# Kernel tuning notes

Measured on AMD Instinct MI355X. Metric: run time of the kernel, lower is better.

The kernel has to match this reference:

```python
import jax, jax.numpy as jnp
import numpy as np

B, N, G = 32, 1024, 8   # batch, Nvecs (= k_in), Nglobals
K_OUT, H = 128, 128     # MLP output width, hidden width
D_IN = 1 + N + G        # MLP input width: [u, norm, dots]


def setup_inputs() -> dict:
    key = jax.random.key(0)
    ks = jax.random.split(key, 8)
    x = jax.random.uniform(ks[0], (B, N, 3), dtype=jnp.float32)  # positive coords -> dots >= 0
    u = jax.random.normal(ks[1], (B, G), dtype=jnp.float32)
    s0 = 1.0 / np.sqrt(D_IN)
    s1 = 1.0 / np.sqrt(H)
    W0 = jax.random.normal(ks[2], (D_IN, H), dtype=jnp.float32) * s0
    b0 = jnp.zeros((H,), dtype=jnp.float32)
    W1 = jax.random.normal(ks[3], (H, H), dtype=jnp.float32) * s1
    b1 = jnp.zeros((H,), dtype=jnp.float32)
    W2 = jax.random.normal(ks[4], (H, K_OUT), dtype=jnp.float32) * s1
    b2 = jnp.zeros((K_OUT,), dtype=jnp.float32)
    return {"x": x, "u": u, "W0": W0, "b0": b0, "W1": W1, "b1": b1, "W2": W2, "b2": b2}


def reference(x, u, W0, b0, W1, b1, W2, b2):
    # x: [B, N, 3], u: [B, G]
    norms = jnp.linalg.norm(x, axis=-1, keepdims=True)            # [B, N, 1]
    dots = jnp.sqrt(jnp.einsum('bid,bjd->bij', x, x))             # [B, N, N]
    u_rep = jnp.broadcast_to(u[:, None, :], (x.shape[0], x.shape[1], u.shape[-1]))
    scalars = jnp.concatenate([u_rep, norms, dots], axis=-1)      # [B, N, G+1+N]
    # MLP (Linear -> LeakyReLU -> Linear -> LeakyReLU -> Linear)
    h = jax.nn.leaky_relu(scalars @ W0 + b0)
    h = jax.nn.leaky_relu(h @ W1 + b1)
    fk = h @ W2 + b2                                              # [B, N, K_OUT]
    # outer product 'bio,bid->biod' followed by mean over i == fused contraction
    out = jnp.einsum('bio,bid->bod', fk, x) / x.shape[1]          # [B, K_OUT, 3]
    return out
```

## Files before the change

kernel.cpp:

```cpp
#include <hip/hip_runtime.h>
#include <hip/hip_fp16.h>

typedef _Float16 f16;
typedef f16 f16x4 __attribute__((ext_vector_type(4)));
typedef f16 f16x8 __attribute__((ext_vector_type(8)));
typedef float f32x4 __attribute__((ext_vector_type(4)));

#define NN 1024

#define IMG2_OFF  0
#define W8_OFF    327680
#define BIAS0_OFF 328192

__global__ __launch_bounds__(256) void prep_kernel(
    const float* __restrict__ u,  const float* __restrict__ W0,
    const float* __restrict__ b0, const float* __restrict__ W1,
    const float* __restrict__ W2,
    f16* __restrict__ img2, float* __restrict__ w8v, float* __restrict__ bias0,
    float* __restrict__ outp)
{
    const int t = threadIdx.x;
    const int blk = blockIdx.x;
    if (blk < 160) {
        int flat = blk * 1024 + t * 4;
        int c   = flat >> 13;
        int rem = flat & 8191;
        int s0  = rem & 7;
        int lm  = (rem >> 3) & 15;
        int q   = (rem >> 7) & 3;
        int ks  = (rem >> 9) & 1;
        int nt  = (rem >> 10) & 3;
        int wn  = (rem >> 12) & 1;
        int n = wn * 64 + nt * 16 + lm;
        f16x4 v;
#pragma unroll
        for (int e = 0; e < 4; ++e) {
            int k = ks * 32 + q * 8 + s0 + e;
            float val;
            if (c < 16)       val = W0[(9 + c * 64 + k) * 128 + n];
            else if (c < 18)  val = W1[((c - 16) * 64 + k) * 128 + n];
            else              val = W2[((c - 18) * 64 + k) * 128 + n];
            v[e] = (f16)val;
        }
        *(f16x4*)&img2[flat] = v;
    } else if (blk < 176) {
        int idx = (blk - 160) * 256 + t;
        int b = idx >> 7, h = idx & 127;
        float s = b0[h];
#pragma unroll
        for (int g = 0; g < 8; ++g) s += u[b * 8 + g] * W0[g * 128 + h];
        bias0[idx] = s;
    } else if (blk == 176) {
        if (t < 128) w8v[t] = W0[8 * 128 + t];
    } else {
        int idx = (blk - 177) * 1024 + t * 4;
        if (idx < 12288) { float4 z = {0.f, 0.f, 0.f, 0.f}; *(float4*)&outp[idx] = z; }
    }
}

__global__ __launch_bounds__(256, 4) void fused_kernel(
    const float* __restrict__ x, const float* __restrict__ b1p,
    const float* __restrict__ b2p, const f16* __restrict__ img2,
    const float* __restrict__ w8v, const float* __restrict__ bias0,
    float* __restrict__ outp)
{
    __shared__ __align__(16) f16 Dsh[2][64 * 64];
    __shared__ __align__(16) f16 xjsh[1024 * 4];
    __shared__ __align__(16) float xi[64 * 4];
    __shared__ float normv[64];
    __shared__ float biass[128];
    __shared__ float w8s[128];

    const int t = threadIdx.x;
    const int b = blockIdx.x >> 4;
    const int i0 = (blockIdx.x & 15) * 64;

    {
        const float* xb = x + (size_t)b * NN * 3;
        float4 v0 = *(const float4*)(xb + t * 12);
        float4 v1 = *(const float4*)(xb + t * 12 + 4);
        float4 v2 = *(const float4*)(xb + t * 12 + 8);
        f16x4 r0; r0[0] = (f16)v0.x; r0[1] = (f16)v0.y; r0[2] = (f16)v0.z; r0[3] = (f16)0;
        f16x4 r1; r1[0] = (f16)v0.w; r1[1] = (f16)v1.x; r1[2] = (f16)v1.y; r1[3] = (f16)0;
        f16x4 r2; r2[0] = (f16)v1.z; r2[1] = (f16)v1.w; r2[2] = (f16)v2.x; r2[3] = (f16)0;
        f16x4 r3; r3[0] = (f16)v2.y; r3[1] = (f16)v2.z; r3[2] = (f16)v2.w; r3[3] = (f16)0;
        *(f16x4*)&xjsh[(t * 4 + 0) * 4] = r0;
        *(f16x4*)&xjsh[(t * 4 + 1) * 4] = r1;
        *(f16x4*)&xjsh[(t * 4 + 2) * 4] = r2;
        *(f16x4*)&xjsh[(t * 4 + 3) * 4] = r3;
    }
    if (t < 192) {
        int i = t / 3, d = t - i * 3;
        xi[i * 4 + d] = x[(size_t)(b * NN + i0 + i) * 3 + d];
    }
    if (t < 128) { biass[t] = bias0[b * 128 + t]; w8s[t] = w8v[t]; }
    __syncthreads();
    if (t < 64) {
        float a0 = xi[t * 4], a1 = xi[t * 4 + 1], a2 = xi[t * 4 + 2];
        normv[t] = __builtin_amdgcn_sqrtf(a0 * a0 + a1 * a1 + a2 * a2);
    }

    const int lane = t & 63, wv = t >> 6;
    const int wm = wv >> 1, wn = wv & 1;
    const int lm = lane & 15, q = lane >> 4;

    f16x4 bi[4];
#pragma unroll
    for (int it = 0; it < 4; ++it) {
        f16x4 v; v[0] = (f16)0; v[1] = (f16)0; v[2] = (f16)0; v[3] = (f16)0;
        if (q == 0) {
            int ii = it * 16 + lm;
            v[0] = (f16)xi[ii * 4];
            v[1] = (f16)xi[ii * 4 + 1];
            v[2] = (f16)xi[ii * 4 + 2];
        }
        bi[it] = v;
    }

    f32x4 acc[2][4];
    auto zero_acc = [&]() {
#pragma unroll
        for (int mt = 0; mt < 2; ++mt)
#pragma unroll
            for (int nt = 0; nt < 4; ++nt)
#pragma unroll
                for (int e = 0; e < 4; ++e) acc[mt][nt][e] = 0.f;
    };
    zero_acc();

    auto dotstore = [&](int jc, int buf) {
        f16x4 ajv; ajv[0] = (f16)0; ajv[1] = (f16)0; ajv[2] = (f16)0; ajv[3] = (f16)0;
        if (q == 0)
            ajv = *(const f16x4*)&xjsh[(jc * 64 + wv * 16 + lm) * 4];
        f32x4 cg[4];
#pragma unroll
        for (int it = 0; it < 4; ++it) {
            f32x4 z; z[0] = 0.f; z[1] = 0.f; z[2] = 0.f; z[3] = 0.f;
            cg[it] = __builtin_amdgcn_mfma_f32_16x16x16f16(ajv, bi[it], z, 0, 0, 0);
        }
#pragma unroll
        for (int it = 0; it < 4; ++it) {
            f16x4 dv;
#pragma unroll
            for (int r = 0; r < 4; ++r)
                dv[r] = (f16)__builtin_amdgcn_sqrtf(fmaxf(cg[it][r], 0.f));
            int row = it * 16 + lm;
            int colstart = wv * 16 + q * 4;
            int addr = row * 64 + (((colstart & ~7) ^ ((row & 7) << 3)) | (colstart & 7));
            *(f16x4*)&Dsh[buf][addr] = dv;
        }
    };

    auto kstep = [&](int dbuf, int c, int dotjc, int dotbuf) {
        f16x8 af[2][2];
#pragma unroll
        for (int mt = 0; mt < 2; ++mt)
#pragma unroll
            for (int ks = 0; ks < 2; ++ks) {
                int row = wm * 32 + mt * 16 + lm;
                int col = ks * 32 + q * 8;
                af[mt][ks] = *(const f16x8*)(Dsh[dbuf] + row * 64 + (col ^ ((row & 7) << 3)));
            }
        const f16* wb = img2 + (size_t)(c * 2 + wn) * 4096 + lane * 8;
        f16x8 bf[4][2];
#pragma unroll
        for (int nt = 0; nt < 4; ++nt)
#pragma unroll
            for (int ks = 0; ks < 2; ++ks)
                bf[nt][ks] = *(const f16x8*)(wb + (nt * 2 + ks) * 512);
        if (dotjc >= 0) dotstore(dotjc, dotbuf);
#pragma unroll
        for (int ks = 0; ks < 2; ++ks)
#pragma unroll
            for (int mt = 0; mt < 2; ++mt)
#pragma unroll
                for (int nt = 0; nt < 4; ++nt)
                    acc[mt][nt] = __builtin_amdgcn_mfma_f32_16x16x32_f16(
                        af[mt][ks], bf[nt][ks], acc[mt][nt], 0, 0, 0);
    };

    dotstore(0, 0);
    __syncthreads();

#pragma unroll
    for (int jc = 0; jc < 16; ++jc) {
        const int cur = jc & 1, nxt = cur ^ 1;
        kstep(cur, jc, (jc < 15) ? jc + 1 : -1, nxt);
        __syncthreads();
    }

#pragma unroll
    for (int mt = 0; mt < 2; ++mt)
#pragma unroll
        for (int nt = 0; nt < 4; ++nt) {
            const int h = wn * 64 + nt * 16 + lm;
            const float bh = biass[h], w8h = w8s[h];
            const int hh = h & 63;
#pragma unroll
            for (int r = 0; r < 4; ++r) {
                int i = wm * 32 + mt * 16 + q * 4 + r;
                float val = acc[mt][nt][r] + bh + normv[i] * w8h;
                val = val > 0.f ? val : 0.01f * val;
                int addr = i * 64 + (((hh & ~7) ^ ((i & 7) << 3)) | (hh & 7));
                Dsh[wn][addr] = (f16)val;
            }
        }
    __syncthreads();

    zero_acc();
    kstep(0, 16, -1, 0);
    kstep(1, 17, -1, 0);
    __syncthreads();

#pragma unroll
    for (int mt = 0; mt < 2; ++mt)
#pragma unroll
        for (int nt = 0; nt < 4; ++nt) {
            const int h = wn * 64 + nt * 16 + lm;
            const float bh = b1p[h];
            const int hh = h & 63;
#pragma unroll
            for (int r = 0; r < 4; ++r) {
                int i = wm * 32 + mt * 16 + q * 4 + r;
                float val = acc[mt][nt][r] + bh;
                val = val > 0.f ? val : 0.01f * val;
                int addr = i * 64 + (((hh & ~7) ^ ((i & 7) << 3)) | (hh & 7));
                Dsh[wn][addr] = (f16)val;
            }
        }
    __syncthreads();

    zero_acc();
    kstep(0, 18, -1, 0);
    kstep(1, 19, -1, 0);

    float p[4][3];
#pragma unroll
    for (int nt = 0; nt < 4; ++nt)
#pragma unroll
        for (int d = 0; d < 3; ++d) p[nt][d] = 0.f;
    float bo[4];
#pragma unroll
    for (int nt = 0; nt < 4; ++nt) bo[nt] = b2p[wn * 64 + nt * 16 + lm];
#pragma unroll
    for (int mt = 0; mt < 2; ++mt)
#pragma unroll
        for (int r = 0; r < 4; ++r) {
            int i = wm * 32 + mt * 16 + q * 4 + r;
            float x0 = xi[i * 4], x1 = xi[i * 4 + 1], x2 = xi[i * 4 + 2];
#pragma unroll
            for (int nt = 0; nt < 4; ++nt) {
                float fkv = acc[mt][nt][r] + bo[nt];
                p[nt][0] = fmaf(fkv, x0, p[nt][0]);
                p[nt][1] = fmaf(fkv, x1, p[nt][1]);
                p[nt][2] = fmaf(fkv, x2, p[nt][2]);
            }
        }
#pragma unroll
    for (int nt = 0; nt < 4; ++nt)
#pragma unroll
        for (int d = 0; d < 3; ++d) {
            float s = p[nt][d];
            s += __shfl_xor(s, 16);
            s += __shfl_xor(s, 32);
            if (q == 0) {
                int o = wn * 64 + nt * 16 + lm;
                atomicAdd(&outp[(b * 128 + o) * 3 + d], s * (1.0f / 1024.0f));
            }
        }
}

extern "C" void kernel_launch(void* const* d_in, const int* in_sizes, int n_in,
                              void* d_out, int out_size, void* d_ws, size_t ws_size,
                              hipStream_t stream) {
    const float* x  = (const float*)d_in[0];
    const float* u  = (const float*)d_in[1];
    const float* W0 = (const float*)d_in[2];
    const float* b0 = (const float*)d_in[3];
    const float* W1 = (const float*)d_in[4];
    const float* b1 = (const float*)d_in[5];
    const float* W2 = (const float*)d_in[6];
    const float* b2 = (const float*)d_in[7];

    char* ws = (char*)d_ws;
    f16*   img2  = (f16*)(ws + IMG2_OFF);
    float* w8v   = (float*)(ws + W8_OFF);
    float* bias0 = (float*)(ws + BIAS0_OFF);
    float* out   = (float*)d_out;

    prep_kernel<<<189, 256, 0, stream>>>(u, W0, b0, W1, W2, img2, w8v, bias0, out);
    fused_kernel<<<512, 256, 0, stream>>>(x, b1, b2, img2, w8v, bias0, out);
}
```

Before: 93.00 us.

## Repartition waves over N, prefetch weight tiles, and keep hidden layers in one LDS tile

Each of the four waves now owns a 32-column slice of the hidden dimension across all 64 rows, instead of a 2x2 grid of 32x64 tiles. Weight fragments for the next j-chunk are double-buffered in registers and loaded before the current MFMAs, and the layer-1/2 weights are loaded before the preceding epilogue. Layers 1 and 2 run as a single K=128 pass over a 64x128 LDS tile rather than two K=64 kstep calls. The aim is to hide global weight-load latency. In exchange the kernel uses more registers, so launch bounds drop to 2 blocks per SIMD, which lowers occupancy.

```diff
diff --git a/kernel.cpp b/kernel.cpp
--- a/kernel.cpp
+++ b/kernel.cpp
@@ -58,7 +58,7 @@
     }
 }
 
-__global__ __launch_bounds__(256, 4) void fused_kernel(
+__global__ __launch_bounds__(256, 2) void fused_kernel(
     const float* __restrict__ x, const float* __restrict__ b1p,
     const float* __restrict__ b2p, const f16* __restrict__ img2,
     const float* __restrict__ w8v, const float* __restrict__ bias0,
@@ -74,6 +74,12 @@
     const int t = threadIdx.x;
     const int b = blockIdx.x >> 4;
     const int i0 = (blockIdx.x & 15) * 64;
+
+    const int lane = t & 63, wv = t >> 6;
+    const int lm = lane & 15, q = lane >> 4;
+    const int half = wv >> 1;
+    const int nbase = (wv & 1) * 2;
+    f16* Hh = &Dsh[0][0];
 
     {
         const float* xb = x + (size_t)b * NN * 3;
@@ -100,10 +106,6 @@
         normv[t] = __builtin_amdgcn_sqrtf(a0 * a0 + a1 * a1 + a2 * a2);
     }
 
-    const int lane = t & 63, wv = t >> 6;
-    const int wm = wv >> 1, wn = wv & 1;
-    const int lm = lane & 15, q = lane >> 4;
-
     f16x4 bi[4];
 #pragma unroll
     for (int it = 0; it < 4; ++it) {
@@ -117,33 +119,18 @@
         bi[it] = v;
     }
 
-    f32x4 acc[2][4];
-    auto zero_acc = [&]() {
-#pragma unroll
-        for (int mt = 0; mt < 2; ++mt)
-#pragma unroll
-            for (int nt = 0; nt < 4; ++nt)
-#pragma unroll
-                for (int e = 0; e < 4; ++e) acc[mt][nt][e] = 0.f;
-    };
-    zero_acc();
-
     auto dotstore = [&](int jc, int buf) {
         f16x4 ajv; ajv[0] = (f16)0; ajv[1] = (f16)0; ajv[2] = (f16)0; ajv[3] = (f16)0;
         if (q == 0)
             ajv = *(const f16x4*)&xjsh[(jc * 64 + wv * 16 + lm) * 4];
-        f32x4 cg[4];
 #pragma unroll
         for (int it = 0; it < 4; ++it) {
             f32x4 z; z[0] = 0.f; z[1] = 0.f; z[2] = 0.f; z[3] = 0.f;
-            cg[it] = __builtin_amdgcn_mfma_f32_16x16x16f16(ajv, bi[it], z, 0, 0, 0);
-        }
-#pragma unroll
-        for (int it = 0; it < 4; ++it) {
+            f32x4 cg = __builtin_amdgcn_mfma_f32_16x16x16f16(ajv, bi[it], z, 0, 0, 0);
             f16x4 dv;
 #pragma unroll
             for (int r = 0; r < 4; ++r)
-                dv[r] = (f16)__builtin_amdgcn_sqrtf(fmaxf(cg[it][r], 0.f));
+                dv[r] = (f16)__builtin_amdgcn_sqrtf(fmaxf(cg[r], 0.f));
             int row = it * 16 + lm;
             int colstart = wv * 16 + q * 4;
             int addr = row * 64 + (((colstart & ~7) ^ ((row & 7) << 3)) | (colstart & 7));
@@ -151,120 +138,187 @@
         }
     };
 
-    auto kstep = [&](int dbuf, int c, int dotjc, int dotbuf) {
-        f16x8 af[2][2];
-#pragma unroll
-        for (int mt = 0; mt < 2; ++mt)
-#pragma unroll
-            for (int ks = 0; ks < 2; ++ks) {
-                int row = wm * 32 + mt * 16 + lm;
-                int col = ks * 32 + q * 8;
-                af[mt][ks] = *(const f16x8*)(Dsh[dbuf] + row * 64 + (col ^ ((row & 7) << 3)));
-            }
-        const f16* wb = img2 + (size_t)(c * 2 + wn) * 4096 + lane * 8;
-        f16x8 bf[4][2];
-#pragma unroll
-        for (int nt = 0; nt < 4; ++nt)
+    f32x4 acc[4][2];
+    auto zero_acc = [&]() {
+#pragma unroll
+        for (int mt = 0; mt < 4; ++mt)
+#pragma unroll
+            for (int n2 = 0; n2 < 2; ++n2)
+#pragma unroll
+                for (int e = 0; e < 4; ++e) acc[mt][n2][e] = 0.f;
+    };
+    zero_acc();
+
+    f16x8 bfbuf[2][2][2];
+    {
+        const f16* wb = img2 + (size_t)(0 * 2 + half) * 4096 + lane * 8;
+#pragma unroll
+        for (int n2 = 0; n2 < 2; ++n2)
 #pragma unroll
             for (int ks = 0; ks < 2; ++ks)
-                bf[nt][ks] = *(const f16x8*)(wb + (nt * 2 + ks) * 512);
-        if (dotjc >= 0) dotstore(dotjc, dotbuf);
-#pragma unroll
-        for (int ks = 0; ks < 2; ++ks)
-#pragma unroll
-            for (int mt = 0; mt < 2; ++mt)
-#pragma unroll
-                for (int nt = 0; nt < 4; ++nt)
-                    acc[mt][nt] = __builtin_amdgcn_mfma_f32_16x16x32_f16(
-                        af[mt][ks], bf[nt][ks], acc[mt][nt], 0, 0, 0);
-    };
-
+                bfbuf[0][n2][ks] = *(const f16x8*)(wb + (((nbase + n2) * 2 + ks)) * 512);
+    }
     dotstore(0, 0);
     __syncthreads();
 
 #pragma unroll
     for (int jc = 0; jc < 16; ++jc) {
         const int cur = jc & 1, nxt = cur ^ 1;
-        kstep(cur, jc, (jc < 15) ? jc + 1 : -1, nxt);
+        if (jc < 15) {
+            const f16* wb = img2 + (size_t)((jc + 1) * 2 + half) * 4096 + lane * 8;
+#pragma unroll
+            for (int n2 = 0; n2 < 2; ++n2)
+#pragma unroll
+                for (int ks = 0; ks < 2; ++ks)
+                    bfbuf[nxt][n2][ks] = *(const f16x8*)(wb + (((nbase + n2) * 2 + ks)) * 512);
+        }
+        f16x8 af[4][2];
+#pragma unroll
+        for (int mt = 0; mt < 4; ++mt)
+#pragma unroll
+            for (int ks = 0; ks < 2; ++ks) {
+                int row = mt * 16 + lm;
+                int col = ks * 32 + q * 8;
+                af[mt][ks] = *(const f16x8*)(Dsh[cur] + row * 64 + (col ^ ((row & 7) << 3)));
+            }
+        if (jc < 15) dotstore(jc + 1, nxt);
+#pragma unroll
+        for (int ks = 0; ks < 2; ++ks)
+#pragma unroll
+            for (int mt = 0; mt < 4; ++mt)
+#pragma unroll
+                for (int n2 = 0; n2 < 2; ++n2)
+                    acc[mt][n2] = __builtin_amdgcn_mfma_f32_16x16x32_f16(
+                        af[mt][ks], bfbuf[cur][n2][ks], acc[mt][n2], 0, 0, 0);
         __syncthreads();
     }
 
-#pragma unroll
-    for (int mt = 0; mt < 2; ++mt)
-#pragma unroll
-        for (int nt = 0; nt < 4; ++nt) {
-            const int h = wn * 64 + nt * 16 + lm;
+    f16x8 bL[2][4];
+#pragma unroll
+    for (int n2 = 0; n2 < 2; ++n2)
+#pragma unroll
+        for (int ks = 0; ks < 4; ++ks) {
+            const f16* wb = img2 + (size_t)((16 + (ks >> 1)) * 2 + half) * 4096 + lane * 8;
+            bL[n2][ks] = *(const f16x8*)(wb + (((nbase + n2) * 2 + (ks & 1))) * 512);
+        }
+
+#pragma unroll
+    for (int mt = 0; mt < 4; ++mt)
+#pragma unroll
+        for (int n2 = 0; n2 < 2; ++n2) {
+            const int h = wv * 32 + n2 * 16 + lm;
             const float bh = biass[h], w8h = w8s[h];
-            const int hh = h & 63;
 #pragma unroll
             for (int r = 0; r < 4; ++r) {
-                int i = wm * 32 + mt * 16 + q * 4 + r;
-                float val = acc[mt][nt][r] + bh + normv[i] * w8h;
+                int i = mt * 16 + q * 4 + r;
+                float val = acc[mt][n2][r] + bh + normv[i] * w8h;
                 val = val > 0.f ? val : 0.01f * val;
-                int addr = i * 64 + (((hh & ~7) ^ ((i & 7) << 3)) | (hh & 7));
-                Dsh[wn][addr] = (f16)val;
+                int addr = i * 128 + (((h & ~7) ^ ((i & 7) << 3)) | (h & 7));
+                Hh[addr] = (f16)val;
             }
         }
     __syncthreads();
 
     zero_acc();
-    kstep(0, 16, -1, 0);
-    kstep(1, 17, -1, 0);
-    __syncthreads();
-
-#pragma unroll
-    for (int mt = 0; mt < 2; ++mt)
-#pragma unroll
-        for (int nt = 0; nt < 4; ++nt) {
-            const int h = wn * 64 + nt * 16 + lm;
+    {
+        f16x8 af[4][4];
+#pragma unroll
+        for (int mt = 0; mt < 4; ++mt)
+#pragma unroll
+            for (int ks = 0; ks < 4; ++ks) {
+                int row = mt * 16 + lm;
+                int col = ks * 32 + q * 8;
+                af[mt][ks] = *(const f16x8*)(Hh + row * 128 + (col ^ ((row & 7) << 3)));
+            }
+#pragma unroll
+        for (int ks = 0; ks < 4; ++ks)
+#pragma unroll
+            for (int mt = 0; mt < 4; ++mt)
+#pragma unroll
+                for (int n2 = 0; n2 < 2; ++n2)
+                    acc[mt][n2] = __builtin_amdgcn_mfma_f32_16x16x32_f16(
+                        af[mt][ks], bL[n2][ks], acc[mt][n2], 0, 0, 0);
+    }
+
+    f16x8 bM[2][4];
+#pragma unroll
+    for (int n2 = 0; n2 < 2; ++n2)
+#pragma unroll
+        for (int ks = 0; ks < 4; ++ks) {
+            const f16* wb = img2 + (size_t)((18 + (ks >> 1)) * 2 + half) * 4096 + lane * 8;
+            bM[n2][ks] = *(const f16x8*)(wb + (((nbase + n2) * 2 + (ks & 1))) * 512);
+        }
+    __syncthreads();
+
+#pragma unroll
+    for (int mt = 0; mt < 4; ++mt)
+#pragma unroll
+        for (int n2 = 0; n2 < 2; ++n2) {
+            const int h = wv * 32 + n2 * 16 + lm;
             const float bh = b1p[h];
-            const int hh = h & 63;
 #pragma unroll
             for (int r = 0; r < 4; ++r) {
-                int i = wm * 32 + mt * 16 + q * 4 + r;
-                float val = acc[mt][nt][r] + bh;
+                int i = mt * 16 + q * 4 + r;
+                float val = acc[mt][n2][r] + bh;
                 val = val > 0.f ? val : 0.01f * val;
-                int addr = i * 64 + (((hh & ~7) ^ ((i & 7) << 3)) | (hh & 7));
-                Dsh[wn][addr] = (f16)val;
+                int addr = i * 128 + (((h & ~7) ^ ((i & 7) << 3)) | (h & 7));
+                Hh[addr] = (f16)val;
             }
         }
     __syncthreads();
 
     zero_acc();
-    kstep(0, 18, -1, 0);
-    kstep(1, 19, -1, 0);
-
-    float p[4][3];
-#pragma unroll
-    for (int nt = 0; nt < 4; ++nt)
-#pragma unroll
-        for (int d = 0; d < 3; ++d) p[nt][d] = 0.f;
-    float bo[4];
-#pragma unroll
-    for (int nt = 0; nt < 4; ++nt) bo[nt] = b2p[wn * 64 + nt * 16 + lm];
-#pragma unroll
-    for (int mt = 0; mt < 2; ++mt)
+    {
+        f16x8 af[4][4];
+#pragma unroll
+        for (int mt = 0; mt < 4; ++mt)
+#pragma unroll
+            for (int ks = 0; ks < 4; ++ks) {
+                int row = mt * 16 + lm;
+                int col = ks * 32 + q * 8;
+                af[mt][ks] = *(const f16x8*)(Hh + row * 128 + (col ^ ((row & 7) << 3)));
+            }
+#pragma unroll
+        for (int ks = 0; ks < 4; ++ks)
+#pragma unroll
+            for (int mt = 0; mt < 4; ++mt)
+#pragma unroll
+                for (int n2 = 0; n2 < 2; ++n2)
+                    acc[mt][n2] = __builtin_amdgcn_mfma_f32_16x16x32_f16(
+                        af[mt][ks], bM[n2][ks], acc[mt][n2], 0, 0, 0);
+    }
+
+    float p[2][3];
+#pragma unroll
+    for (int n2 = 0; n2 < 2; ++n2)
+#pragma unroll
+        for (int d = 0; d < 3; ++d) p[n2][d] = 0.f;
+    float bo[2];
+#pragma unroll
+    for (int n2 = 0; n2 < 2; ++n2) bo[n2] = b2p[wv * 32 + n2 * 16 + lm];
+#pragma unroll
+    for (int mt = 0; mt < 4; ++mt)
 #pragma unroll
         for (int r = 0; r < 4; ++r) {
-            int i = wm * 32 + mt * 16 + q * 4 + r;
+            int i = mt * 16 + q * 4 + r;
             float x0 = xi[i * 4], x1 = xi[i * 4 + 1], x2 = xi[i * 4 + 2];
 #pragma unroll
-            for (int nt = 0; nt < 4; ++nt) {
-                float fkv = acc[mt][nt][r] + bo[nt];
-                p[nt][0] = fmaf(fkv, x0, p[nt][0]);
-                p[nt][1] = fmaf(fkv, x1, p[nt][1]);
-                p[nt][2] = fmaf(fkv, x2, p[nt][2]);
-            }
-        }
-#pragma unroll
-    for (int nt = 0; nt < 4; ++nt)
+            for (int n2 = 0; n2 < 2; ++n2) {
+                float fkv = acc[mt][n2][r] + bo[n2];
+                p[n2][0] = fmaf(fkv, x0, p[n2][0]);
+                p[n2][1] = fmaf(fkv, x1, p[n2][1]);
+                p[n2][2] = fmaf(fkv, x2, p[n2][2]);
+            }
+        }
+#pragma unroll
+    for (int n2 = 0; n2 < 2; ++n2)
 #pragma unroll
         for (int d = 0; d < 3; ++d) {
-            float s = p[nt][d];
+            float s = p[n2][d];
             s += __shfl_xor(s, 16);
             s += __shfl_xor(s, 32);
             if (q == 0) {
-                int o = wn * 64 + nt * 16 + lm;
+                int o = wv * 32 + n2 * 16 + lm;
                 atomicAdd(&outp[(b * 128 + o) * 3 + d], s * (1.0f / 1024.0f));
             }
         }
```

Measured after the change: 85.44 us. 1.09x faster.

## Give each wave private dot tiles to remove per-chunk block barriers

Applied to the files above, without the earlier changes.

Each wave now computes its own 32x64 slice of sqrt-dot values into a private double-buffered shared tile, so the 16-step main K loop needs no __syncthreads. B-operand weight fragments are register double-buffered one chunk ahead, and the layer 2/3 weights are preloaded before the barriers. The cost is redundant dot-product MFMAs (each wave computes all 64 j columns for its 32 rows), a larger shared footprint, higher register pressure, and occupancy lowered from 4 to 3 blocks per CU.

```diff
diff --git a/kernel.cpp b/kernel.cpp
--- a/kernel.cpp
+++ b/kernel.cpp
@@ -58,13 +58,13 @@
     }
 }
 
-__global__ __launch_bounds__(256, 4) void fused_kernel(
+__global__ __launch_bounds__(256, 3) void fused_kernel(
     const float* __restrict__ x, const float* __restrict__ b1p,
     const float* __restrict__ b2p, const f16* __restrict__ img2,
     const float* __restrict__ w8v, const float* __restrict__ bias0,
     float* __restrict__ outp)
 {
-    __shared__ __align__(16) f16 Dsh[2][64 * 64];
+    __shared__ __align__(16) f16 Dsh[4][2][32 * 64];
     __shared__ __align__(16) f16 xjsh[1024 * 4];
     __shared__ __align__(16) float xi[64 * 4];
     __shared__ float normv[64];
@@ -74,6 +74,12 @@
     const int t = threadIdx.x;
     const int b = blockIdx.x >> 4;
     const int i0 = (blockIdx.x & 15) * 64;
+
+    const int lane = t & 63, wv = t >> 6;
+    const int lm = lane & 15, q = lane >> 4;
+    const int ih = wv >> 1;
+    const int hh = wv & 1;
+    f16* Hh = &Dsh[0][0][0];
 
     {
         const float* xb = x + (size_t)b * NN * 3;
@@ -99,17 +105,14 @@
         float a0 = xi[t * 4], a1 = xi[t * 4 + 1], a2 = xi[t * 4 + 2];
         normv[t] = __builtin_amdgcn_sqrtf(a0 * a0 + a1 * a1 + a2 * a2);
     }
-
-    const int lane = t & 63, wv = t >> 6;
-    const int wm = wv >> 1, wn = wv & 1;
-    const int lm = lane & 15, q = lane >> 4;
-
-    f16x4 bi[4];
-#pragma unroll
-    for (int it = 0; it < 4; ++it) {
+    __syncthreads();
+
+    f16x4 bi[2];
+#pragma unroll
+    for (int it = 0; it < 2; ++it) {
         f16x4 v; v[0] = (f16)0; v[1] = (f16)0; v[2] = (f16)0; v[3] = (f16)0;
         if (q == 0) {
-            int ii = it * 16 + lm;
+            int ii = ih * 32 + it * 16 + lm;
             v[0] = (f16)xi[ii * 4];
             v[1] = (f16)xi[ii * 4 + 1];
             v[2] = (f16)xi[ii * 4 + 2];
@@ -117,6 +120,28 @@
         bi[it] = v;
     }
 
+    auto dotstore = [&](int jc, int par) {
+#pragma unroll
+        for (int g = 0; g < 4; ++g) {
+            f16x4 ajv; ajv[0] = (f16)0; ajv[1] = (f16)0; ajv[2] = (f16)0; ajv[3] = (f16)0;
+            if (q == 0)
+                ajv = *(const f16x4*)&xjsh[(jc * 64 + g * 16 + lm) * 4];
+#pragma unroll
+            for (int it = 0; it < 2; ++it) {
+                f32x4 z; z[0] = 0.f; z[1] = 0.f; z[2] = 0.f; z[3] = 0.f;
+                f32x4 cg = __builtin_amdgcn_mfma_f32_16x16x16f16(ajv, bi[it], z, 0, 0, 0);
+                f16x4 dv;
+#pragma unroll
+                for (int r = 0; r < 4; ++r)
+                    dv[r] = (f16)__builtin_amdgcn_sqrtf(fmaxf(cg[r], 0.f));
+                int row = it * 16 + lm;
+                int col0 = g * 16 + q * 4;
+                int addr = row * 64 + (((col0 & ~7) ^ ((row & 7) << 3)) | (col0 & 7));
+                *(f16x4*)&Dsh[wv][par][addr] = dv;
+            }
+        }
+    };
+
     f32x4 acc[2][4];
     auto zero_acc = [&]() {
 #pragma unroll
@@ -128,47 +153,33 @@
     };
     zero_acc();
 
-    auto dotstore = [&](int jc, int buf) {
-        f16x4 ajv; ajv[0] = (f16)0; ajv[1] = (f16)0; ajv[2] = (f16)0; ajv[3] = (f16)0;
-        if (q == 0)
-            ajv = *(const f16x4*)&xjsh[(jc * 64 + wv * 16 + lm) * 4];
-        f32x4 cg[4];
-#pragma unroll
-        for (int it = 0; it < 4; ++it) {
-            f32x4 z; z[0] = 0.f; z[1] = 0.f; z[2] = 0.f; z[3] = 0.f;
-            cg[it] = __builtin_amdgcn_mfma_f32_16x16x16f16(ajv, bi[it], z, 0, 0, 0);
-        }
-#pragma unroll
-        for (int it = 0; it < 4; ++it) {
-            f16x4 dv;
-#pragma unroll
-            for (int r = 0; r < 4; ++r)
-                dv[r] = (f16)__builtin_amdgcn_sqrtf(fmaxf(cg[it][r], 0.f));
-            int row = it * 16 + lm;
-            int colstart = wv * 16 + q * 4;
-            int addr = row * 64 + (((colstart & ~7) ^ ((row & 7) << 3)) | (colstart & 7));
-            *(f16x4*)&Dsh[buf][addr] = dv;
-        }
+    f16x8 bfbuf[2][4][2];
+    auto loadB = [&](int c, int par) {
+        const f16* wb = img2 + (size_t)(c * 2 + hh) * 4096 + lane * 8;
+#pragma unroll
+        for (int nt = 0; nt < 4; ++nt)
+#pragma unroll
+            for (int ks = 0; ks < 2; ++ks)
+                bfbuf[par][nt][ks] = *(const f16x8*)(wb + (nt * 2 + ks) * 512);
     };
 
-    auto kstep = [&](int dbuf, int c, int dotjc, int dotbuf) {
+    loadB(0, 0);
+    dotstore(0, 0);
+
+#pragma unroll 2
+    for (int jc = 0; jc < 16; ++jc) {
+        const int cur = jc & 1, nxt = cur ^ 1;
+        if (jc < 15) loadB(jc + 1, nxt);
         f16x8 af[2][2];
 #pragma unroll
         for (int mt = 0; mt < 2; ++mt)
 #pragma unroll
             for (int ks = 0; ks < 2; ++ks) {
-                int row = wm * 32 + mt * 16 + lm;
+                int row = mt * 16 + lm;
                 int col = ks * 32 + q * 8;
-                af[mt][ks] = *(const f16x8*)(Dsh[dbuf] + row * 64 + (col ^ ((row & 7) << 3)));
-            }
-        const f16* wb = img2 + (size_t)(c * 2 + wn) * 4096 + lane * 8;
-        f16x8 bf[4][2];
-#pragma unroll
-        for (int nt = 0; nt < 4; ++nt)
-#pragma unroll
-            for (int ks = 0; ks < 2; ++ks)
-                bf[nt][ks] = *(const f16x8*)(wb + (nt * 2 + ks) * 512);
-        if (dotjc >= 0) dotstore(dotjc, dotbuf);
+                af[mt][ks] = *(const f16x8*)(Dsh[wv][cur] + row * 64 + (col ^ ((row & 7) << 3)));
+            }
+        if (jc < 15) dotstore(jc + 1, nxt);
 #pragma unroll
         for (int ks = 0; ks < 2; ++ks)
 #pragma unroll
@@ -176,63 +187,98 @@
 #pragma unroll
                 for (int nt = 0; nt < 4; ++nt)
                     acc[mt][nt] = __builtin_amdgcn_mfma_f32_16x16x32_f16(
-                        af[mt][ks], bf[nt][ks], acc[mt][nt], 0, 0, 0);
-    };
-
-    dotstore(0, 0);
-    __syncthreads();
-
-#pragma unroll
-    for (int jc = 0; jc < 16; ++jc) {
-        const int cur = jc & 1, nxt = cur ^ 1;
-        kstep(cur, jc, (jc < 15) ? jc + 1 : -1, nxt);
-        __syncthreads();
-    }
+                        af[mt][ks], bfbuf[cur][nt][ks], acc[mt][nt], 0, 0, 0);
+    }
+
+    f16x8 bL[4][4];
+#pragma unroll
+    for (int nt = 0; nt < 4; ++nt)
+#pragma unroll
+        for (int kk = 0; kk < 4; ++kk) {
+            const f16* wb = img2 + (size_t)((16 + (kk >> 1)) * 2 + hh) * 4096 + lane * 8;
+            bL[nt][kk] = *(const f16x8*)(wb + (nt * 2 + (kk & 1)) * 512);
+        }
+    __syncthreads();
 
 #pragma unroll
     for (int mt = 0; mt < 2; ++mt)
 #pragma unroll
         for (int nt = 0; nt < 4; ++nt) {
-            const int h = wn * 64 + nt * 16 + lm;
+            const int h = hh * 64 + nt * 16 + lm;
             const float bh = biass[h], w8h = w8s[h];
-            const int hh = h & 63;
 #pragma unroll
             for (int r = 0; r < 4; ++r) {
-                int i = wm * 32 + mt * 16 + q * 4 + r;
+                int i = ih * 32 + mt * 16 + q * 4 + r;
                 float val = acc[mt][nt][r] + bh + normv[i] * w8h;
                 val = val > 0.f ? val : 0.01f * val;
-                int addr = i * 64 + (((hh & ~7) ^ ((i & 7) << 3)) | (hh & 7));
-                Dsh[wn][addr] = (f16)val;
+                int addr = i * 128 + (((h & ~7) ^ ((i & 7) << 3)) | (h & 7));
+                Hh[addr] = (f16)val;
             }
         }
     __syncthreads();
 
     zero_acc();
-    kstep(0, 16, -1, 0);
-    kstep(1, 17, -1, 0);
+#pragma unroll
+    for (int kk = 0; kk < 4; ++kk) {
+        f16x8 af[2];
+#pragma unroll
+        for (int mt = 0; mt < 2; ++mt) {
+            int row = ih * 32 + mt * 16 + lm;
+            int col = kk * 32 + q * 8;
+            af[mt] = *(const f16x8*)(Hh + row * 128 + (col ^ ((row & 7) << 3)));
+        }
+#pragma unroll
+        for (int mt = 0; mt < 2; ++mt)
+#pragma unroll
+            for (int nt = 0; nt < 4; ++nt)
+                acc[mt][nt] = __builtin_amdgcn_mfma_f32_16x16x32_f16(
+                    af[mt], bL[nt][kk], acc[mt][nt], 0, 0, 0);
+    }
+
+    f16x8 bM[4][4];
+#pragma unroll
+    for (int nt = 0; nt < 4; ++nt)
+#pragma unroll
+        for (int kk = 0; kk < 4; ++kk) {
+            const f16* wb = img2 + (size_t)((18 + (kk >> 1)) * 2 + hh) * 4096 + lane * 8;
+            bM[nt][kk] = *(const f16x8*)(wb + (nt * 2 + (kk & 1)) * 512);
+        }
     __syncthreads();
 
 #pragma unroll
     for (int mt = 0; mt < 2; ++mt)
 #pragma unroll
         for (int nt = 0; nt < 4; ++nt) {
-            const int h = wn * 64 + nt * 16 + lm;
+            const int h = hh * 64 + nt * 16 + lm;
             const float bh = b1p[h];
-            const int hh = h & 63;
 #pragma unroll
             for (int r = 0; r < 4; ++r) {
-                int i = wm * 32 + mt * 16 + q * 4 + r;
+                int i = ih * 32 + mt * 16 + q * 4 + r;
                 float val = acc[mt][nt][r] + bh;
                 val = val > 0.f ? val : 0.01f * val;
-                int addr = i * 64 + (((hh & ~7) ^ ((i & 7) << 3)) | (hh & 7));
-                Dsh[wn][addr] = (f16)val;
+                int addr = i * 128 + (((h & ~7) ^ ((i & 7) << 3)) | (h & 7));
+                Hh[addr] = (f16)val;
             }
         }
     __syncthreads();
 
     zero_acc();
-    kstep(0, 18, -1, 0);
-    kstep(1, 19, -1, 0);
+#pragma unroll
+    for (int kk = 0; kk < 4; ++kk) {
+        f16x8 af[2];
+#pragma unroll
+        for (int mt = 0; mt < 2; ++mt) {
+            int row = ih * 32 + mt * 16 + lm;
+            int col = kk * 32 + q * 8;
+            af[mt] = *(const f16x8*)(Hh + row * 128 + (col ^ ((row & 7) << 3)));
+        }
+#pragma unroll
+        for (int mt = 0; mt < 2; ++mt)
+#pragma unroll
+            for (int nt = 0; nt < 4; ++nt)
+                acc[mt][nt] = __builtin_amdgcn_mfma_f32_16x16x32_f16(
+                    af[mt], bM[nt][kk], acc[mt][nt], 0, 0, 0);
+    }
 
     float p[4][3];
 #pragma unroll
@@ -241,12 +287,12 @@
         for (int d = 0; d < 3; ++d) p[nt][d] = 0.f;
     float bo[4];
 #pragma unroll
-    for (int nt = 0; nt < 4; ++nt) bo[nt] = b2p[wn * 64 + nt * 16 + lm];
+    for (int nt = 0; nt < 4; ++nt) bo[nt] = b2p[hh * 64 + nt * 16 + lm];
 #pragma unroll
     for (int mt = 0; mt < 2; ++mt)
 #pragma unroll
         for (int r = 0; r < 4; ++r) {
-            int i = wm * 32 + mt * 16 + q * 4 + r;
+            int i = ih * 32 + mt * 16 + q * 4 + r;
             float x0 = xi[i * 4], x1 = xi[i * 4 + 1], x2 = xi[i * 4 + 2];
 #pragma unroll
             for (int nt = 0; nt < 4; ++nt) {
@@ -264,7 +310,7 @@
             s += __shfl_xor(s, 16);
             s += __shfl_xor(s, 32);
             if (q == 0) {
-                int o = wn * 64 + nt * 16 + lm;
+                int o = hh * 64 + nt * 16 + lm;
                 atomicAdd(&outp[(b * 128 + o) * 3 + d], s * (1.0f / 1024.0f));
             }
         }
```

Result: slower. 95.50 us (+2.7%).
